# Kernel optimization log

Measured on AMD Instinct MI355X. Metric: run time of the kernel, lower is better.

## Reference

```python
import jax, jax.numpy as jnp
import numpy as np

B, L, T, LM, DFF, D, H = 8, 256, 2048, 4096, 1024, 84, 4
HD = D // H  # 21
NCLS = 265


def _ln(x, s, b):
    m = x.mean(-1, keepdims=True)
    v = ((x - m) ** 2).mean(-1, keepdims=True)
    return (x - m) * jax.lax.rsqrt(v + 1e-5) * s + b


def _fourier(xyz, gB):
    # PositionEmbeddingCoordsSine(d_pos=10, pos_type='fourier'): xyz @ B * 2pi -> [sin, cos]
    proj = (2.0 * jnp.pi) * jnp.einsum('bnc,cd->bnd', xyz, gB)  # [B,N,5]
    return jnp.concatenate([jnp.sin(proj), jnp.cos(proj)], axis=-1)  # [B,N,10]


def setup_inputs() -> dict:
    key = jax.random.key(0)
    ks = jax.random.split(key, 20)
    def nrm(k, shape, scale):
        return jax.random.normal(k, shape, jnp.float32) * scale
    coords = jax.random.uniform(ks[0], (B, L, 6), jnp.float32)
    cls = jax.random.randint(ks[1], (B, L), 0, NCLS).astype(jnp.float32)
    vision_features = jnp.concatenate([coords, cls[..., None]], axis=-1)  # [B,L,7]
    FIN = D * L + LM  # 25600
    inp = {
        'grd_tokens': nrm(ks[2], (T, LM), 1.0),
        'vision_features': vision_features,
        'token_batch_idx': jax.random.randint(ks[3], (T,), 0, B),
        'gauss_B': nrm(ks[4], (3, 5), 1.0),
        'class_emb': nrm(ks[5], (NCLS, 64), 0.02),
        'w_in': nrm(ks[6], (2, D, 3 * D), D ** -0.5),
        'b_in': jnp.zeros((2, 3 * D), jnp.float32),
        'w_out': nrm(ks[7], (2, D, D), D ** -0.5),
        'b_out': jnp.zeros((2, D), jnp.float32),
        'ln1_s': jnp.ones((2, D), jnp.float32), 'ln1_b': jnp.zeros((2, D), jnp.float32),
        'w_ff1': nrm(ks[8], (2, D, DFF), D ** -0.5), 'b_ff1': jnp.zeros((2, DFF), jnp.float32),
        'w_ff2': nrm(ks[9], (2, DFF, D), DFF ** -0.5), 'b_ff2': jnp.zeros((2, D), jnp.float32),
        'ln2_s': jnp.ones((2, D), jnp.float32), 'ln2_b': jnp.zeros((2, D), jnp.float32),
        'w0': nrm(ks[10], (FIN, DFF), FIN ** -0.5), 'b0': jnp.zeros((DFF,), jnp.float32),
        'w1': nrm(ks[11], (DFF, DFF), DFF ** -0.5), 'b1': jnp.zeros((DFF,), jnp.float32),
        'w2': nrm(ks[12], (DFF, DFF), DFF ** -0.5), 'b2': jnp.zeros((DFF,), jnp.float32),
        'w3': nrm(ks[13], (DFF, DFF), DFF ** -0.5), 'b3': jnp.zeros((DFF,), jnp.float32),
        'w4': nrm(ks[14], (DFF, 6), DFF ** -0.5), 'b4': jnp.zeros((6,), jnp.float32),
    }
    return inp


def reference(grd_tokens, vision_features, token_batch_idx, gauss_B, class_emb,
              w_in, b_in, w_out, b_out, ln1_s, ln1_b, w_ff1, b_ff1, w_ff2, b_ff2,
              ln2_s, ln2_b, w0, b0, w1, b1, w2, b2, w3, b3, w4, b4):
    pe_min = _fourier(vision_features[:, :, 0:3], gauss_B)  # [B,L,10]
    pe_max = _fourier(vision_features[:, :, 3:6], gauss_B)  # [B,L,10]
    cls = vision_features[:, :, -1].astype(jnp.int32)
    src = jnp.concatenate([pe_min, pe_max, class_emb[cls]], axis=-1)  # [B,L,84]
    pad = jnp.all(vision_features == 0, axis=-1)  # [B,L]
    neg = jnp.where(pad, -1e9, 0.0)[:, None, None, :]  # [B,1,1,L] key-padding bias
    # 2-layer post-norm transformer encoder (DETR-style, pos=None, dropout=0)
    for l in range(2):
        qkv = src @ w_in[l] + b_in[l]
        q, k, v = jnp.split(qkv, 3, axis=-1)
        q = q.reshape(B, L, H, HD)
        k = k.reshape(B, L, H, HD)
        v = v.reshape(B, L, H, HD)
        scores = jnp.einsum('blhd,bmhd->bhlm', q, k) / jnp.sqrt(jnp.float32(HD)) + neg
        attn = jax.nn.softmax(scores, axis=-1)
        o = jnp.einsum('bhlm,bmhd->blhd', attn, v).reshape(B, L, D)
        src = _ln(src + o @ w_out[l] + b_out[l], ln1_s[l], ln1_b[l])
        ff = jax.nn.relu(src @ w_ff1[l] + b_ff1[l]) @ w_ff2[l] + b_ff2[l]
        src = _ln(src + ff, ln2_s[l], ln2_b[l])
    vision_flat = src.reshape(B, L * D)  # flattened encoder output per sample [B, 21504]
    # batched version of the ragged python loop: gather per-token vision feat + concat lm feat
    feat = jnp.concatenate([vision_flat[token_batch_idx], grd_tokens], axis=-1)  # [T, 25600]
    h = jax.nn.relu(feat @ w0 + b0)
    h = jax.nn.relu(h @ w1 + b1)
    h = jax.nn.relu(h @ w2 + b2)
    h = jax.nn.relu(h @ w3 + b3)
    return h @ w4 + b4  # [T, 6]
```

## Files before the change

### kernel.cpp

```cpp
#include <hip/hip_runtime.h>
#include <hip/hip_bf16.h>

#define B_ 8
#define L_ 256
#define T_ 2048
#define LM_ 4096
#define DFF_ 1024
#define D_ 84
#define H_ 4
#define HD_ 21
#define BL_ (B_*L_)
#define VISF_ (L_*D_)
#define VKS 168
#define VCHUNK (VISF_/VKS)
#define AKS 8
#define AKEYS (L_/AKS)

typedef __attribute__((ext_vector_type(8))) short bf16x8;
typedef __attribute__((ext_vector_type(4))) float f32x4;

typedef const __attribute__((address_space(1))) int* gas_p;
typedef __attribute__((address_space(3))) int* las_p;
__device__ __forceinline__ void gld_lds16(const void* g, void* l) {
    __builtin_amdgcn_global_load_lds((gas_p)g, (las_p)l, 16, 0, 0);
}

__global__ void k_build_src(const float* __restrict__ vf, const float* __restrict__ gB,
                            const float* __restrict__ cemb, float* __restrict__ src,
                            float* __restrict__ neg)
{
    int row = blockIdx.x * blockDim.x + threadIdx.x;
    if (row >= BL_) return;
    float v[7];
    bool allz = true;
    #pragma unroll
    for (int c = 0; c < 7; ++c) { v[c] = vf[row*7 + c]; allz = allz && (v[c] == 0.0f); }
    neg[row] = allz ? -1e9f : 0.0f;
    float* s = src + (size_t)row * D_;
    const float TWO_PI = 6.28318530717958647692f;
    #pragma unroll
    for (int d = 0; d < 5; ++d) {
        float pmin = TWO_PI * (v[0]*gB[d] + v[1]*gB[5+d] + v[2]*gB[10+d]);
        float pmax = TWO_PI * (v[3]*gB[d] + v[4]*gB[5+d] + v[5]*gB[10+d]);
        s[d]      = sinf(pmin);  s[5+d]  = cosf(pmin);
        s[10+d]   = sinf(pmax);  s[15+d] = cosf(pmax);
    }
    int cls = (int)v[6];
    const float4* ce = reinterpret_cast<const float4*>(cemb + (size_t)cls*64);
    float4* so = reinterpret_cast<float4*>(s + 20);
    #pragma unroll
    for (int i = 0; i < 16; ++i) so[i] = ce[i];
}

__global__ __launch_bounds__(256) void k_qkv8(const float* __restrict__ src,
        const float* __restrict__ w_in, const float* __restrict__ b_in,
        float* __restrict__ qkv, int lay)
{
    __shared__ float s8[8][D_];
    int r0 = blockIdx.x * 8, tid = threadIdx.x;
    for (int idx = tid; idx < 8*D_; idx += 256) {
        int r = idx / D_, d = idx - r*D_;
        s8[r][d] = src[(size_t)(r0+r)*D_ + d];
    }
    __syncthreads();
    if (tid < 3*D_) {
        const float* w = w_in + (size_t)lay*D_*3*D_ + tid;
        float acc[8] = {};
        for (int d = 0; d < D_; ++d) {
            float wv = w[(size_t)d*3*D_];
            #pragma unroll
            for (int r = 0; r < 8; ++r) acc[r] = fmaf(s8[r][d], wv, acc[r]);
        }
        float bv = b_in[lay*3*D_ + tid];
        #pragma unroll
        for (int r = 0; r < 8; ++r) qkv[(size_t)(r0+r)*(3*D_) + tid] = acc[r] + bv;
    }
}

__global__ __launch_bounds__(256) void k_attn_part(const float* __restrict__ qkv,
        const float* __restrict__ neg, float* __restrict__ part)
{
    __shared__ float ks_[AKEYS*HD_], vs_[AKEYS*HD_], ns[AKEYS];
    int bh = blockIdx.x;
    int b = bh >> 2, h = bh & 3;
    int sp = blockIdx.y;
    int tid = threadIdx.x;
    int k0 = sp * AKEYS;
    for (int idx = tid; idx < AKEYS*HD_; idx += 256) {
        int l = idx / HD_, d = idx - l*HD_;
        size_t base = ((size_t)(b*L_ + k0 + l))*(3*D_) + h*HD_ + d;
        ks_[idx] = qkv[base + D_];
        vs_[idx] = qkv[base + 2*D_];
    }
    if (tid < AKEYS) ns[tid] = neg[b*L_ + k0 + tid];
    __syncthreads();
    float q[HD_];
    {
        size_t base = ((size_t)(b*L_ + tid))*(3*D_) + h*HD_;
        #pragma unroll
        for (int d = 0; d < HD_; ++d) q[d] = qkv[base + d];
    }
    const float scale = 0.21821789023599239f;
    float m_run = -INFINITY, l_run = 0.0f;
    float o[HD_];
    #pragma unroll
    for (int d = 0; d < HD_; ++d) o[d] = 0.0f;
    for (int m = 0; m < AKEYS; ++m) {
        const float* krow = &ks_[m*HD_];
        float sdot = 0.0f;
        #pragma unroll
        for (int d = 0; d < HD_; ++d) sdot = fmaf(q[d], krow[d], sdot);
        float sc = sdot * scale + ns[m];
        float nm = fmaxf(m_run, sc);
        float c = __expf(m_run - nm);
        float p = __expf(sc - nm);
        l_run = l_run * c + p;
        const float* vrow = &vs_[m*HD_];
        #pragma unroll
        for (int d = 0; d < HD_; ++d) o[d] = fmaf(p, vrow[d], o[d]*c);
        m_run = nm;
    }
    float* po = part + (((size_t)bh*AKS + sp)*L_ + tid)*24;
    #pragma unroll
    for (int d = 0; d < HD_; ++d) po[d] = o[d];
    po[21] = m_run;
    po[22] = l_run;
}

__global__ __launch_bounds__(64) void k_attn_merge(const float* __restrict__ part,
        float* __restrict__ attn_o)
{
    int bh = blockIdx.x;
    int b = bh >> 2, h = bh & 3;
    int q = blockIdx.y*64 + threadIdx.x;
    const float* pb = part + ((size_t)bh*AKS*L_ + q)*24;
    float m_tot = -INFINITY;
    #pragma unroll
    for (int sp = 0; sp < AKS; ++sp)
        m_tot = fmaxf(m_tot, pb[(size_t)sp*L_*24 + 21]);
    float l_tot = 0.0f;
    float o[HD_];
    #pragma unroll
    for (int d = 0; d < HD_; ++d) o[d] = 0.0f;
    #pragma unroll
    for (int sp = 0; sp < AKS; ++sp) {
        const float* pp = pb + (size_t)sp*L_*24;
        float e = __expf(pp[21] - m_tot);
        l_tot = fmaf(pp[22], e, l_tot);
        #pragma unroll
        for (int d = 0; d < HD_; ++d) o[d] = fmaf(pp[d], e, o[d]);
    }
    float inv = 1.0f / l_tot;
    float* op = attn_o + ((size_t)(b*L_ + q))*D_ + h*HD_;
    #pragma unroll
    for (int d = 0; d < HD_; ++d) op[d] = o[d]*inv;
}

__global__ __launch_bounds__(128) void k_oproj_ln(const float* __restrict__ attn_o,
        const float* __restrict__ w_out, const float* __restrict__ b_out,
        const float* __restrict__ ln_s, const float* __restrict__ ln_b,
        float* __restrict__ src, __hip_bfloat16* __restrict__ srcb, int lay)
{
    __shared__ float os[D_];
    __shared__ float r1[128], r2[128];
    int row = blockIdx.x, tid = threadIdx.x;
    if (tid < D_) os[tid] = attn_o[(size_t)row*D_ + tid];
    __syncthreads();
    float y = 0.0f;
    if (tid < D_) {
        const float* w = w_out + (size_t)lay*D_*D_ + tid;
        float acc = b_out[lay*D_ + tid];
        for (int d = 0; d < D_; ++d) acc = fmaf(os[d], w[(size_t)d*D_], acc);
        y = src[(size_t)row*D_ + tid] + acc;
    }
    r1[tid] = (tid < D_) ? y : 0.0f;
    r2[tid] = (tid < D_) ? y*y : 0.0f;
    __syncthreads();
    for (int s = 64; s > 0; s >>= 1) {
        if (tid < s) { r1[tid] += r1[tid+s]; r2[tid] += r2[tid+s]; }
        __syncthreads();
    }
    float mean = r1[0] * (1.0f/D_);
    float var  = r2[0] * (1.0f/D_) - mean*mean;
    float rstd = rsqrtf(var + 1e-5f);
    float out = 0.0f;
    if (tid < D_) {
        out = (y - mean)*rstd*ln_s[lay*D_+tid] + ln_b[lay*D_+tid];
        src[(size_t)row*D_ + tid] = out;
    }
    srcb[(size_t)row*128 + tid] = (tid < D_) ? __float2bfloat16(out)
                                             : __float2bfloat16(0.0f);
}

__global__ __launch_bounds__(256) void k_ff2_mfma(
        const __hip_bfloat16* __restrict__ hb,
        const __hip_bfloat16* __restrict__ wt,
        float* __restrict__ part)
{
    __shared__ __align__(16) __hip_bfloat16 sA[2][4096];
    __shared__ __align__(16) __hip_bfloat16 sB[2][6144];
    int tid = threadIdx.x;
    int bm = blockIdx.x * 64, sp = blockIdx.y;
    int wave = tid >> 6, lane = tid & 63;
    int wr = wave >> 1, wc = wave & 1;
    int l15 = lane & 15, l4 = lane >> 4;
    f32x4 acc[2][3] = {};

    const int a_m0 = tid & 63;
    const int b_i0 = tid,       b_kb0 = b_i0/96, b_n0 = b_i0%96;
    const int b_i1 = tid + 256, b_kb1 = b_i1/96, b_n1 = b_i1%96;
    const int b_i2 = tid + 512, b_kb2 = b_i2/96, b_n2 = b_i2%96;
    const __hip_bfloat16* Ap0 = hb + (size_t)(bm + a_m0)*1024 + sp*128 + (tid>>6)*8;
    const __hip_bfloat16* Ap1 = Ap0 + 32;
    const __hip_bfloat16* Bp0 = wt + (size_t)b_n0*1024 + sp*128 + b_kb0*8;
    const __hip_bfloat16* Bp1 = wt + (size_t)b_n1*1024 + sp*128 + b_kb1*8;
    const __hip_bfloat16* Bp2 = wt + (size_t)b_n2*1024 + sp*128 + b_kb2*8;

    gld_lds16(Ap0, (char*)&sA[0][0] + tid*16);
    gld_lds16(Ap1, (char*)&sA[0][0] + (tid+256)*16);
    gld_lds16(Bp0, (char*)&sB[0][0] + b_i0*16);
    gld_lds16(Bp1, (char*)&sB[0][0] + b_i1*16);
    gld_lds16(Bp2, (char*)&sB[0][0] + b_i2*16);
    #pragma unroll
    for (int t = 0; t < 2; ++t) {
        __syncthreads();
        if (t == 0) {
            gld_lds16(Ap0 + 64, (char*)&sA[1][0] + tid*16);
            gld_lds16(Ap1 + 64, (char*)&sA[1][0] + (tid+256)*16);
            gld_lds16(Bp0 + 64, (char*)&sB[1][0] + b_i0*16);
            gld_lds16(Bp1 + 64, (char*)&sB[1][0] + b_i1*16);
            gld_lds16(Bp2 + 64, (char*)&sB[1][0] + b_i2*16);
        }
        const __hip_bfloat16* sa = &sA[t][0];
        const __hip_bfloat16* sb = &sB[t][0];
        #pragma unroll
        for (int ks = 0; ks < 2; ++ks) {
            bf16x8 af[2], bfr[3];
            #pragma unroll
            for (int mi = 0; mi < 2; ++mi)
                af[mi] = *reinterpret_cast<const bf16x8*>(
                    &sa[(size_t)((ks*4 + l4)*64 + wr*32 + mi*16 + l15) * 8]);
            #pragma unroll
            for (int ni = 0; ni < 3; ++ni)
                bfr[ni] = *reinterpret_cast<const bf16x8*>(
                    &sb[(size_t)((ks*4 + l4)*96 + wc*48 + ni*16 + l15) * 8]);
            #pragma unroll
            for (int mi = 0; mi < 2; ++mi)
                #pragma unroll
                for (int ni = 0; ni < 3; ++ni)
                    acc[mi][ni] = __builtin_amdgcn_mfma_f32_16x16x32_bf16(
                        af[mi], bfr[ni], acc[mi][ni], 0, 0, 0);
        }
    }
    float* po = part + (size_t)sp*(2048*96);
    #pragma unroll
    for (int mi = 0; mi < 2; ++mi)
        #pragma unroll
        for (int reg = 0; reg < 4; ++reg) {
            int row = bm + wr*32 + mi*16 + l4*4 + reg;
            #pragma unroll
            for (int ni = 0; ni < 3; ++ni) {
                int col = wc*48 + ni*16 + l15;
                po[(size_t)row*96 + col] = acc[mi][ni][reg];
            }
        }
}

__global__ __launch_bounds__(128) void k_ff2ln_red(const float* __restrict__ part,
        const float* __restrict__ b_ff2, const float* __restrict__ ln_s,
        const float* __restrict__ ln_b, float* __restrict__ src, int lay)
{
    __shared__ float r1[128], r2[128];
    int row = blockIdx.x, tid = threadIdx.x;
    float y = 0.0f;
    if (tid < D_) {
        #pragma unroll
        for (int sp = 0; sp < 8; ++sp)
            y += part[(size_t)sp*(2048*96) + (size_t)row*96 + tid];
        y += b_ff2[lay*D_ + tid] + src[(size_t)row*D_ + tid];
    }
    r1[tid] = (tid < D_) ? y : 0.0f;
    r2[tid] = (tid < D_) ? y*y : 0.0f;
    __syncthreads();
    for (int s = 64; s > 0; s >>= 1) {
        if (tid < s) { r1[tid] += r1[tid+s]; r2[tid] += r2[tid+s]; }
        __syncthreads();
    }
    float mean = r1[0] * (1.0f/D_);
    float var  = r2[0] * (1.0f/D_) - mean*mean;
    float rstd = rsqrtf(var + 1e-5f);
    if (tid < D_)
        src[(size_t)row*D_ + tid] = (y - mean)*rstd*ln_s[lay*D_+tid] + ln_b[lay*D_+tid];
}

__global__ __launch_bounds__(256) void k_vis_gemm(const float* __restrict__ src,
        const float* __restrict__ w0, float* __restrict__ partials)
{
    __shared__ float vf[8][VCHUNK];
    __shared__ float red[8][256][4];
    int nt = blockIdx.x, sp = blockIdx.y, tid = threadIdx.x;
    int k0 = sp * VCHUNK;
    for (int idx = tid; idx < 8*VCHUNK; idx += 256) {
        int r = idx >> 7, c = idx & 127;
        vf[r][c] = src[(size_t)r*VISF_ + k0 + c];
    }
    __syncthreads();
    int ng = tid & 31;
    int kh = tid >> 5;
    const float* wp = w0 + (size_t)(k0 + kh*16)*DFF_ + nt*128 + ng*4;
    float acc[8][4] = {};
    #pragma unroll 4
    for (int kk = 0; kk < 16; ++kk) {
        float4 w = *reinterpret_cast<const float4*>(wp + (size_t)kk*DFF_);
        #pragma unroll
        for (int m = 0; m < 8; ++m) {
            float sv = vf[m][kh*16 + kk];
            acc[m][0] = fmaf(sv, w.x, acc[m][0]);
            acc[m][1] = fmaf(sv, w.y, acc[m][1]);
            acc[m][2] = fmaf(sv, w.z, acc[m][2]);
            acc[m][3] = fmaf(sv, w.w, acc[m][3]);
        }
    }
    #pragma unroll
    for (int m = 0; m < 8; ++m)
        *reinterpret_cast<float4*>(&red[m][tid][0]) =
            make_float4(acc[m][0], acc[m][1], acc[m][2], acc[m][3]);
    __syncthreads();
    int m2 = tid >> 5, ng2 = tid & 31;
    float4 s = *reinterpret_cast<const float4*>(&red[m2][ng2][0]);
    #pragma unroll
    for (int j = 1; j < 8; ++j) {
        float4 v = *reinterpret_cast<const float4*>(&red[m2][j*32 + ng2][0]);
        s.x += v.x; s.y += v.y; s.z += v.z; s.w += v.w;
    }
    *reinterpret_cast<float4*>(
        &partials[(size_t)sp*8192 + m2*1024 + nt*128 + ng2*4]) = s;
}

__global__ __launch_bounds__(256) void k_vis_red1(const float* __restrict__ partials,
        float* __restrict__ p2)
{
    int o = blockIdx.x*256 + threadIdx.x;
    int g = blockIdx.y;
    float s = 0.0f;
    #pragma unroll
    for (int j = 0; j < 14; ++j) s += partials[(size_t)(g*14 + j)*8192 + o];
    p2[(size_t)g*8192 + o] = s;
}

__global__ __launch_bounds__(256) void k_vis_red2(const float* __restrict__ p2,
        float* __restrict__ vis)
{
    int o = blockIdx.x*256 + threadIdx.x;
    float s = 0.0f;
    #pragma unroll
    for (int g = 0; g < 12; ++g) s += p2[(size_t)g*8192 + o];
    vis[o] = s;
}

struct bh4 { __hip_bfloat16 x, y, z, w; };

__global__ __launch_bounds__(256) void k_f2b(const float* __restrict__ in,
        __hip_bfloat16* __restrict__ out, int n4)
{
    int i = blockIdx.x*256 + threadIdx.x;
    if (i >= n4) return;
    float4 v = reinterpret_cast<const float4*>(in)[i];
    bh4 o = { __float2bfloat16(v.x), __float2bfloat16(v.y),
              __float2bfloat16(v.z), __float2bfloat16(v.w) };
    reinterpret_cast<bh4*>(out)[i] = o;
}

__global__ __launch_bounds__(256) void k_wT(const float* __restrict__ W,
        __hip_bfloat16* __restrict__ WT, int K, int N)
{
    __shared__ float t[32][33];
    int kb = blockIdx.x*32, nb = blockIdx.y*32;
    int tx = threadIdx.x & 31, ty = threadIdx.x >> 5;
    #pragma unroll
    for (int i = 0; i < 4; ++i)
        t[ty + i*8][tx] = W[(size_t)(kb + ty + i*8)*N + nb + tx];
    __syncthreads();
    #pragma unroll
    for (int i = 0; i < 4; ++i)
        WT[(size_t)(nb + ty + i*8)*K + kb + tx] = __float2bfloat16(t[tx][ty + i*8]);
}

__global__ __launch_bounds__(256) void k_wTp(const float* __restrict__ W,
        __hip_bfloat16* __restrict__ WT, int K, int N, int KP)
{
    __shared__ float t[32][33];
    int kb = blockIdx.x*32, nb = blockIdx.y*32;
    int tx = threadIdx.x & 31, ty = threadIdx.x >> 5;
    #pragma unroll
    for (int i = 0; i < 4; ++i) {
        int k = kb + ty + i*8, n = nb + tx;
        t[ty + i*8][tx] = (k < K && n < N) ? W[(size_t)k*N + n] : 0.0f;
    }
    __syncthreads();
    #pragma unroll
    for (int i = 0; i < 4; ++i)
        WT[(size_t)(nb + ty + i*8)*KP + kb + tx] = __float2bfloat16(t[tx][ty + i*8]);
}

template<bool ADD_VIS>
__global__ __launch_bounds__(256) void mfma_gemm(
        const __hip_bfloat16* __restrict__ A,
        const __hip_bfloat16* __restrict__ WT,
        const float* __restrict__ bias,
        const float* __restrict__ vis,
        const int* __restrict__ bidx,
        __hip_bfloat16* __restrict__ C,
        int K)
{
    constexpr int N = 1024;
    __shared__ __align__(16) __hip_bfloat16 sA[3][4096];
    __shared__ __align__(16) __hip_bfloat16 sB[3][4096];
    int tid = threadIdx.x;
    int bm = blockIdx.x * 64, bn = blockIdx.y * 64;
    int wave = tid >> 6, lane = tid & 63;
    int wr = wave >> 1, wc = wave & 1;
    int l15 = lane & 15, l4 = lane >> 4;
    f32x4 acc[2][2] = {};

    const __hip_bfloat16* Ap = A  + (size_t)(bm + (tid & 63))*K + (tid >> 6)*8;
    const __hip_bfloat16* Bp = WT + (size_t)(bn + (tid & 63))*K + (tid >> 6)*8;

    int nsteps = K >> 6;
    auto STAGE = [&](int t, int b) {
        int ko = t << 6;
        char* la = (char*)&sA[b][0];
        char* lb = (char*)&sB[b][0];
        gld_lds16(Ap + ko,      la + tid*16);
        gld_lds16(Ap + ko + 32, la + (tid+256)*16);
        gld_lds16(Bp + ko,      lb + tid*16);
        gld_lds16(Bp + ko + 32, lb + (tid+256)*16);
    };
    STAGE(0, 0);
    if (nsteps > 1) STAGE(1, 1);

    for (int t = 0; t < nsteps; ++t) {
        if (t + 2 < nsteps) {
            STAGE(t + 2, (t + 2) % 3);
            asm volatile("s_waitcnt vmcnt(8)" ::: "memory");
        } else if (t + 1 < nsteps) {
            asm volatile("s_waitcnt vmcnt(4)" ::: "memory");
        } else {
            asm volatile("s_waitcnt vmcnt(0)" ::: "memory");
        }
        __builtin_amdgcn_s_barrier();
        const __hip_bfloat16* sa = &sA[t % 3][0];
        const __hip_bfloat16* sb = &sB[t % 3][0];
        #pragma unroll
        for (int ks = 0; ks < 2; ++ks) {
            bf16x8 af[2], bfr[2];
            #pragma unroll
            for (int mi = 0; mi < 2; ++mi)
                af[mi] = *reinterpret_cast<const bf16x8*>(
                    &sa[(size_t)((ks*4 + l4)*64 + wr*32 + mi*16 + l15) * 8]);
            #pragma unroll
            for (int ni = 0; ni < 2; ++ni)
                bfr[ni] = *reinterpret_cast<const bf16x8*>(
                    &sb[(size_t)((ks*4 + l4)*64 + wc*32 + ni*16 + l15) * 8]);
            #pragma unroll
            for (int mi = 0; mi < 2; ++mi)
                #pragma unroll
                for (int ni = 0; ni < 2; ++ni)
                    acc[mi][ni] = __builtin_amdgcn_mfma_f32_16x16x32_bf16(
                        af[mi], bfr[ni], acc[mi][ni], 0, 0, 0);
        }
        __builtin_amdgcn_s_barrier();
    }

    #pragma unroll
    for (int mi = 0; mi < 2; ++mi) {
        #pragma unroll
        for (int reg = 0; reg < 4; ++reg) {
            int row = bm + wr*32 + mi*16 + l4*4 + reg;
            const float* vrow = nullptr;
            if (ADD_VIS) vrow = vis + (size_t)bidx[row]*1024;
            #pragma unroll
            for (int ni = 0; ni < 2; ++ni) {
                int col = bn + wc*32 + ni*16 + l15;
                float v = acc[mi][ni][reg] + bias[col];
                if (ADD_VIS) v += vrow[col];
                v = fmaxf(v, 0.0f);
                C[(size_t)row*N + col] = __float2bfloat16(v);
            }
        }
    }
}

__global__ __launch_bounds__(64) void k_final(const __hip_bfloat16* __restrict__ h,
        const float* __restrict__ w4, const float* __restrict__ b4, float* __restrict__ out)
{
    int t = blockIdx.x, lane = threadIdx.x;
    float acc[6] = {};
    for (int k = lane; k < DFF_; k += 64) {
        float hv = __bfloat162float(h[(size_t)t*DFF_ + k]);
        #pragma unroll
        for (int j = 0; j < 6; ++j) acc[j] = fmaf(hv, w4[k*6 + j], acc[j]);
    }
    #pragma unroll
    for (int j = 0; j < 6; ++j)
        #pragma unroll
        for (int s = 32; s > 0; s >>= 1) acc[j] += __shfl_down(acc[j], s);
    if (lane == 0) {
        #pragma unroll
        for (int j = 0; j < 6; ++j) out[(size_t)t*6 + j] = acc[j] + b4[j];
    }
}

extern "C" void kernel_launch(void* const* d_in, const int* in_sizes, int n_in,
                              void* d_out, int out_size, void* d_ws, size_t ws_size,
                              hipStream_t stream)
{
    const float* grd   = (const float*)d_in[0];
    const float* vfeat = (const float*)d_in[1];
    const int*   tbi   = (const int*)  d_in[2];
    const float* gB    = (const float*)d_in[3];
    const float* cemb  = (const float*)d_in[4];
    const float* w_in  = (const float*)d_in[5];
    const float* b_in  = (const float*)d_in[6];
    const float* w_out = (const float*)d_in[7];
    const float* b_out = (const float*)d_in[8];
    const float* ln1_s = (const float*)d_in[9];
    const float* ln1_b = (const float*)d_in[10];
    const float* w_ff1 = (const float*)d_in[11];
    const float* b_ff1 = (const float*)d_in[12];
    const float* w_ff2 = (const float*)d_in[13];
    const float* b_ff2 = (const float*)d_in[14];
    const float* ln2_s = (const float*)d_in[15];
    const float* ln2_b = (const float*)d_in[16];
    const float* w0    = (const float*)d_in[17];
    const float* b0    = (const float*)d_in[18];
    const float* w1    = (const float*)d_in[19];
    const float* b1    = (const float*)d_in[20];
    const float* w2    = (const float*)d_in[21];
    const float* b2    = (const float*)d_in[22];
    const float* w3    = (const float*)d_in[23];
    const float* b3    = (const float*)d_in[24];
    const float* w4    = (const float*)d_in[25];
    const float* b4    = (const float*)d_in[26];

    float* ws = (float*)d_ws;
    float* src    = ws;
    float* neg    = src    + 172032;
    float* qkv    = neg    + 2048;
    float* attn_o = qkv    + 516096;
    float* vparts = attn_o + 172032;
    float* vp2    = vparts + 1376256;
    float* visp   = vp2    + 98304;
    float* ffpart = visp   + 8192;
    float* fend   = ffpart + 1572864;
    __hip_bfloat16* grdb  = (__hip_bfloat16*)fend;
    __hip_bfloat16* w0t   = grdb  + 8388608;
    __hip_bfloat16* w1t   = w0t   + 4194304;
    __hip_bfloat16* w2t   = w1t   + 1048576;
    __hip_bfloat16* w3t   = w2t   + 1048576;
    __hip_bfloat16* hab   = w3t   + 1048576;
    __hip_bfloat16* hbb   = hab   + 2097152;
    __hip_bfloat16* srcb  = hbb   + 2097152;
    __hip_bfloat16* wff1t = srcb  + 262144;
    __hip_bfloat16* wff2t = wff1t + 262144;
    __hip_bfloat16* ffh   = hab;

    k_f2b<<<(T_*LM_/4 + 255)/256, 256, 0, stream>>>(grd, grdb, T_*LM_/4);
    k_wT<<<dim3(LM_/32,  DFF_/32), 256, 0, stream>>>(w0 + (size_t)VISF_*DFF_, w0t, LM_,  DFF_);
    k_wT<<<dim3(DFF_/32, DFF_/32), 256, 0, stream>>>(w1, w1t, DFF_, DFF_);
    k_wT<<<dim3(DFF_/32, DFF_/32), 256, 0, stream>>>(w2, w2t, DFF_, DFF_);
    k_wT<<<dim3(DFF_/32, DFF_/32), 256, 0, stream>>>(w3, w3t, DFF_, DFF_);
    for (int l = 0; l < 2; ++l) {
        k_wTp<<<dim3(128/32, 1024/32), 256, 0, stream>>>(
            w_ff1 + (size_t)l*D_*DFF_, wff1t + (size_t)l*1024*128, D_, DFF_, 128);
        k_wTp<<<dim3(1024/32, 96/32),  256, 0, stream>>>(
            w_ff2 + (size_t)l*DFF_*D_, wff2t + (size_t)l*96*1024, DFF_, D_, 1024);
    }

    k_build_src<<<8, 256, 0, stream>>>(vfeat, gB, cemb, src, neg);

    for (int lay = 0; lay < 2; ++lay) {
        k_qkv8      <<<BL_/8, 256, 0, stream>>>(src, w_in, b_in, qkv, lay);
        k_attn_part <<<dim3(B_*H_, AKS), 256, 0, stream>>>(qkv, neg, ffpart);
        k_attn_merge<<<dim3(B_*H_, 4), 64, 0, stream>>>(ffpart, attn_o);
        k_oproj_ln  <<<BL_, 128, 0, stream>>>(attn_o, w_out, b_out, ln1_s, ln1_b, src, srcb, lay);
        mfma_gemm<false><<<dim3(32, 16), 256, 0, stream>>>(
            srcb, wff1t + (size_t)lay*1024*128, b_ff1 + lay*DFF_,
            nullptr, nullptr, ffh, 128);
        k_ff2_mfma<<<dim3(32, 8), 256, 0, stream>>>(
            ffh, wff2t + (size_t)lay*96*1024, ffpart);
        k_ff2ln_red<<<BL_, 128, 0, stream>>>(ffpart, b_ff2, ln2_s, ln2_b, src, lay);
    }

    k_vis_gemm<<<dim3(8, VKS), 256, 0, stream>>>(src, w0, vparts);
    k_vis_red1<<<dim3(32, 12), 256, 0, stream>>>(vparts, vp2);
    k_vis_red2<<<32, 256, 0, stream>>>(vp2, visp);

    dim3 mg(T_/64, DFF_/64);
    mfma_gemm<true ><<<mg, 256, 0, stream>>>(grdb, w0t, b0, visp, tbi, hab, LM_);
    mfma_gemm<false><<<mg, 256, 0, stream>>>(hab,  w1t, b1, nullptr, nullptr, hbb, DFF_);
    mfma_gemm<false><<<mg, 256, 0, stream>>>(hbb,  w2t, b2, nullptr, nullptr, hab, DFF_);
    mfma_gemm<false><<<mg, 256, 0, stream>>>(hab,  w3t, b3, nullptr, nullptr, hbb, DFF_);

    k_final<<<T_, 64, 0, stream>>>(hbb, w4, b4, (float*)d_out);
}
```

Before: 290.3 us.

## Split-K the head MLP GEMMs in two with separate reduce-epilogue kernels

The four head GEMMs (2048x1024 outputs) now split K into two slices, which doubles the grid from 512 to 1024 workgroups to fill more CUs on the MI355X. Each slice writes fp32 partials to a new workspace buffer. A separate elementwise kernel sums the two partials and applies bias, the optional per-token vision add, ReLU and the bf16 conversion. In exchange each layer gains an extra launch and a round trip of about 16 MB of fp32 partials through memory.

```diff
diff --git a/kernel.cpp b/kernel.cpp
--- a/kernel.cpp
+++ b/kernel.cpp
@@ -405,13 +405,9 @@
 
 template<bool ADD_VIS>
 __global__ __launch_bounds__(256) void mfma_gemm(
-        const __hip_bfloat16* __restrict__ A,
-        const __hip_bfloat16* __restrict__ WT,
-        const float* __restrict__ bias,
-        const float* __restrict__ vis,
-        const int* __restrict__ bidx,
-        __hip_bfloat16* __restrict__ C,
-        int K)
+        const __hip_bfloat16* __restrict__ A, const __hip_bfloat16* __restrict__ WT,
+        const float* __restrict__ bias, const float* __restrict__ vis,
+        const int* __restrict__ bidx, __hip_bfloat16* __restrict__ C, int K)
 {
     constexpr int N = 1024;
     __shared__ __align__(16) __hip_bfloat16 sA[3][4096];
@@ -489,6 +485,107 @@
             }
         }
     }
+}
+
+__global__ __launch_bounds__(256) void mfma_gemm_ks(
+        const __hip_bfloat16* __restrict__ A,
+        const __hip_bfloat16* __restrict__ WT,
+        float* __restrict__ part,
+        int K, int kslice)
+{
+    constexpr int N = 1024;
+    __shared__ __align__(16) __hip_bfloat16 sA[3][4096];
+    __shared__ __align__(16) __hip_bfloat16 sB[3][4096];
+    int tid = threadIdx.x;
+    int bm = blockIdx.x * 64, bn = blockIdx.y * 64, z = blockIdx.z;
+    int wave = tid >> 6, lane = tid & 63;
+    int wr = wave >> 1, wc = wave & 1;
+    int l15 = lane & 15, l4 = lane >> 4;
+    f32x4 acc[2][2] = {};
+
+    const __hip_bfloat16* Ap = A  + (size_t)(bm + (tid & 63))*K + z*kslice + (tid >> 6)*8;
+    const __hip_bfloat16* Bp = WT + (size_t)(bn + (tid & 63))*K + z*kslice + (tid >> 6)*8;
+
+    int nsteps = kslice >> 6;
+    auto STAGE = [&](int t, int b) {
+        int ko = t << 6;
+        char* la = (char*)&sA[b][0];
+        char* lb = (char*)&sB[b][0];
+        gld_lds16(Ap + ko,      la + tid*16);
+        gld_lds16(Ap + ko + 32, la + (tid+256)*16);
+        gld_lds16(Bp + ko,      lb + tid*16);
+        gld_lds16(Bp + ko + 32, lb + (tid+256)*16);
+    };
+    STAGE(0, 0);
+    if (nsteps > 1) STAGE(1, 1);
+
+    for (int t = 0; t < nsteps; ++t) {
+        if (t + 2 < nsteps) {
+            STAGE(t + 2, (t + 2) % 3);
+            asm volatile("s_waitcnt vmcnt(8)" ::: "memory");
+        } else if (t + 1 < nsteps) {
+            asm volatile("s_waitcnt vmcnt(4)" ::: "memory");
+        } else {
+            asm volatile("s_waitcnt vmcnt(0)" ::: "memory");
+        }
+        __builtin_amdgcn_s_barrier();
+        const __hip_bfloat16* sa = &sA[t % 3][0];
+        const __hip_bfloat16* sb = &sB[t % 3][0];
+        #pragma unroll
+        for (int ks = 0; ks < 2; ++ks) {
+            bf16x8 af[2], bfr[2];
+            #pragma unroll
+            for (int mi = 0; mi < 2; ++mi)
+                af[mi] = *reinterpret_cast<const bf16x8*>(
+                    &sa[(size_t)((ks*4 + l4)*64 + wr*32 + mi*16 + l15) * 8]);
+            #pragma unroll
+            for (int ni = 0; ni < 2; ++ni)
+                bfr[ni] = *reinterpret_cast<const bf16x8*>(
+                    &sb[(size_t)((ks*4 + l4)*64 + wc*32 + ni*16 + l15) * 8]);
+            #pragma unroll
+            for (int mi = 0; mi < 2; ++mi)
+                #pragma unroll
+                for (int ni = 0; ni < 2; ++ni)
+                    acc[mi][ni] = __builtin_amdgcn_mfma_f32_16x16x32_bf16(
+                        af[mi], bfr[ni], acc[mi][ni], 0, 0, 0);
+        }
+        __builtin_amdgcn_s_barrier();
+    }
+
+    float* po = part + (size_t)z*(T_*DFF_);
+    #pragma unroll
+    for (int mi = 0; mi < 2; ++mi)
+        #pragma unroll
+        for (int reg = 0; reg < 4; ++reg) {
+            int row = bm + wr*32 + mi*16 + l4*4 + reg;
+            #pragma unroll
+            for (int ni = 0; ni < 2; ++ni) {
+                int col = bn + wc*32 + ni*16 + l15;
+                po[(size_t)row*N + col] = acc[mi][ni][reg];
+            }
+        }
+}
+
+template<bool ADD_VIS>
+__global__ __launch_bounds__(256) void k_head_red(const float* __restrict__ part,
+        const float* __restrict__ bias, const float* __restrict__ vis,
+        const int* __restrict__ bidx, __hip_bfloat16* __restrict__ C)
+{
+    int o = (blockIdx.x*256 + threadIdx.x) * 4;
+    int row = o >> 10, col = o & 1023;
+    float4 a = *reinterpret_cast<const float4*>(&part[o]);
+    float4 b = *reinterpret_cast<const float4*>(&part[o + (size_t)T_*DFF_]);
+    float4 bb = *reinterpret_cast<const float4*>(&bias[col]);
+    float vx = 0.f, vy = 0.f, vz = 0.f, vw = 0.f;
+    if (ADD_VIS) {
+        float4 v = *reinterpret_cast<const float4*>(&vis[(size_t)bidx[row]*1024 + col]);
+        vx = v.x; vy = v.y; vz = v.z; vw = v.w;
+    }
+    bh4 out = { __float2bfloat16(fmaxf(a.x + b.x + bb.x + vx, 0.0f)),
+                __float2bfloat16(fmaxf(a.y + b.y + bb.y + vy, 0.0f)),
+                __float2bfloat16(fmaxf(a.z + b.z + bb.z + vz, 0.0f)),
+                __float2bfloat16(fmaxf(a.w + b.w + bb.w + vw, 0.0f)) };
+    *reinterpret_cast<bh4*>(&C[o]) = out;
 }
 
 __global__ __launch_bounds__(64) void k_final(const __hip_bfloat16* __restrict__ h,
@@ -552,7 +649,8 @@
     float* vp2    = vparts + 1376256;
     float* visp   = vp2    + 98304;
     float* ffpart = visp   + 8192;
-    float* fend   = ffpart + 1572864;
+    float* gpart  = ffpart + 1572864;
+    float* fend   = gpart  + 4194304;
     __hip_bfloat16* grdb  = (__hip_bfloat16*)fend;
     __hip_bfloat16* w0t   = grdb  + 8388608;
     __hip_bfloat16* w1t   = w0t   + 4194304;
@@ -596,11 +694,15 @@
     k_vis_red1<<<dim3(32, 12), 256, 0, stream>>>(vparts, vp2);
     k_vis_red2<<<32, 256, 0, stream>>>(vp2, visp);
 
-    dim3 mg(T_/64, DFF_/64);
-    mfma_gemm<true ><<<mg, 256, 0, stream>>>(grdb, w0t, b0, visp, tbi, hab, LM_);
-    mfma_gemm<false><<<mg, 256, 0, stream>>>(hab,  w1t, b1, nullptr, nullptr, hbb, DFF_);
-    mfma_gemm<false><<<mg, 256, 0, stream>>>(hbb,  w2t, b2, nullptr, nullptr, hab, DFF_);
-    mfma_gemm<false><<<mg, 256, 0, stream>>>(hab,  w3t, b3, nullptr, nullptr, hbb, DFF_);
+    dim3 rg(T_*DFF_/1024);
+    mfma_gemm_ks<<<dim3(32, 16, 2), 256, 0, stream>>>(grdb, w0t, gpart, LM_, LM_/2);
+    k_head_red<true ><<<rg, 256, 0, stream>>>(gpart, b0, visp, tbi, hab);
+    mfma_gemm_ks<<<dim3(32, 16, 2), 256, 0, stream>>>(hab, w1t, gpart, DFF_, DFF_/2);
+    k_head_red<false><<<rg, 256, 0, stream>>>(gpart, b1, nullptr, nullptr, hbb);
+    mfma_gemm_ks<<<dim3(32, 16, 2), 256, 0, stream>>>(hbb, w2t, gpart, DFF_, DFF_/2);
+    k_head_red<false><<<rg, 256, 0, stream>>>(gpart, b2, nullptr, nullptr, hab);
+    mfma_gemm_ks<<<dim3(32, 16, 2), 256, 0, stream>>>(hab, w3t, gpart, DFF_, DFF_/2);
+    k_head_red<false><<<rg, 256, 0, stream>>>(gpart, b3, nullptr, nullptr, hbb);
 
     k_final<<<T_, 64, 0, stream>>>(hbb, w4, b4, (float*)d_out);
 }
```

Result: slower. 327.0 us (+12.7%).
